# Optimization experiments

Measured on AMD Instinct MI355X. Metric: run time of the kernel, lower is better.

## Reference

```python
import jax, jax.numpy as jnp
import numpy as np

H, KB = 8, 8          # z_num grid (h, k)
OB, IB = 64, 64       # per-call weight block [OB, IB, K]
K, L = 9, 9           # kernel dims of exe_unet_weight and unet_1d_weights
ZD, PD, DH = 64, 16, 128  # z_dim, pde_inputs dim, hypernet hidden


def setup_inputs() -> dict:
    key = jax.random.key(0)
    k1, k2, k3, k4, k5 = jax.random.split(key, 5)
    # z params: torch.fmod(randn, 2) as in the original __init__
    z_all = jnp.fmod(jax.random.normal(k1, (H * KB, ZD), jnp.float32), 2.0)
    W1 = jax.random.normal(k2, (DH, ZD + PD), jnp.float32) * 0.1
    b1 = jnp.zeros((DH,), jnp.float32)
    W2 = jax.random.normal(k3, (OB * IB * K, DH), jnp.float32) * 0.02
    b2 = jnp.zeros((OB * IB * K,), jnp.float32)
    unet_1d_weights = jax.random.normal(k4, (H * OB, KB * IB, L), jnp.float32)
    pde_inputs = jax.random.normal(k5, (PD,), jnp.float32)
    return {"z_all": z_all, "W1": W1, "b1": b1, "W2": W2, "b2": b2,
            "unet_1d_weights": unet_1d_weights, "pde_inputs": pde_inputs}


def reference(z_all, W1, b1, W2, b2, unet_1d_weights, pde_inputs):
    # Batched hypernet: one GEMM over all h*k z vectors instead of h*k calls.
    x = jnp.concatenate([z_all, jnp.broadcast_to(pde_inputs, (H * KB, PD))], axis=1)  # [hk, ZD+PD]
    hid = jax.nn.relu(x @ W1.T + b1)                    # [hk, DH]
    w = (hid @ W2.T + b2).reshape(H, KB, OB, IB, K)      # per-cell blocks
    # cat(dim=1) within row, cat(dim=0) across rows -> [H*OB, KB*IB, K]
    exe_unet_weight = w.transpose(0, 2, 1, 3, 4).reshape(H * OB, KB * IB, K)
    # broadcast outer product over kernel dims
    w_2d = jnp.einsum('oik,oil->oikl', exe_unet_weight, unet_1d_weights)
    return w_2d
```

## Files before the change

kernel.cpp:

```cpp
#include <hip/hip_runtime.h>

#define ZD_ 64
#define PD_ 16
#define DH_ 128

__global__ void hid_kernel(const float* __restrict__ z_all,
                           const float* __restrict__ W1,
                           const float* __restrict__ b1,
                           const float* __restrict__ pde,
                           float* __restrict__ hid) {
    int gid = blockIdx.x * 256 + threadIdx.x;
    int r = gid >> 7;
    int d = gid & 127;
    const float* w = W1 + d * (ZD_ + PD_);
    const float* z = z_all + r * ZD_;
    float acc = b1[d];
    #pragma unroll 8
    for (int c = 0; c < ZD_; ++c) acc += z[c] * w[c];
    #pragma unroll
    for (int c = 0; c < PD_; ++c) acc += pde[c] * w[ZD_ + c];
    hid[gid] = fmaxf(acc, 0.0f);
}

__global__ __launch_bounds__(256, 4) void fused_kernel(
        const float* __restrict__ hid,
        const float* __restrict__ W2,
        const float* __restrict__ b2,
        const float* __restrict__ unet,
        float* __restrict__ out) {
    __shared__ __align__(16) float s_w2[36 * 132];
    __shared__ float s_exe[64 * 36];
    __shared__ float s_un [64 * 36];

    int tid = threadIdx.x;
    int b   = blockIdx.x;
    int ob  = b >> 4;
    int ibg = b & 15;
    int n0  = ob * 576 + ibg * 36;

    const float4* g4 = reinterpret_cast<const float4*>(W2 + (size_t)n0 * DH_);
    for (int j = tid; j < 1152; j += 256) {
        int row  = j >> 5;
        int col4 = j & 31;
        *reinterpret_cast<float4*>(&s_w2[row * 132 + col4 * 4]) = g4[j];
    }

    for (int idx = tid; idx < 2304; idx += 256) {
        int rr = idx / 36;
        int jj = idx - rr * 36;
        int h  = rr >> 3, kb = rr & 7;
        size_t ub = ((size_t)((h * 64 + ob) * 512 + kb * 64 + ibg * 4)) * 9;
        s_un[idx] = unet[ub + jj];
    }
    __syncthreads();

    int cell = tid >> 2;
    int ib   = tid & 3;
    const float4* h4p = reinterpret_cast<const float4*>(hid + cell * DH_);
    const float*  wb  = s_w2 + ib * 9 * 132;
    const float*  bp  = b2 + n0 + ib * 9;

    float acc[9];
    #pragma unroll
    for (int k = 0; k < 9; ++k) acc[k] = bp[k];

    #pragma unroll 4
    for (int c = 0; c < 32; ++c) {
        float4 h4 = h4p[c];
        #pragma unroll
        for (int k = 0; k < 9; ++k) {
            float4 w4 = *reinterpret_cast<const float4*>(wb + k * 132 + c * 4);
            acc[k] += h4.x * w4.x + h4.y * w4.y + h4.z * w4.z + h4.w * w4.w;
        }
    }
    #pragma unroll
    for (int k = 0; k < 9; ++k) s_exe[tid * 9 + k] = acc[k];
    __syncthreads();

    for (int idx = tid; idx < 5184; idx += 256) {
        int rr = idx / 81;
        int q  = idx - rr * 81;
        float4 v;
        float* vp = &v.x;
        #pragma unroll
        for (int j2 = 0; j2 < 4; ++j2) {
            int e   = q * 4 + j2;
            int ibb = e / 81;
            int rem = e - ibb * 81;
            int k   = rem / 9;
            int l   = rem - k * 9;
            vp[j2] = s_exe[rr * 36 + ibb * 9 + k] * s_un[rr * 36 + ibb * 9 + l];
        }
        int h = rr >> 3, kb = rr & 7;
        size_t base = ((size_t)((h * 64 + ob) * 512 + kb * 64 + ibg * 4)) * 81;
        reinterpret_cast<float4*>(out + base)[q] = v;
    }
}

extern "C" void kernel_launch(void* const* d_in, const int* in_sizes, int n_in,
                              void* d_out, int out_size, void* d_ws, size_t ws_size,
                              hipStream_t stream) {
    const float* z_all = (const float*)d_in[0];
    const float* W1    = (const float*)d_in[1];
    const float* b1    = (const float*)d_in[2];
    const float* W2    = (const float*)d_in[3];
    const float* b2    = (const float*)d_in[4];
    const float* unet  = (const float*)d_in[5];
    const float* pde   = (const float*)d_in[6];
    float* out = (float*)d_out;

    float* hid = (float*)d_ws;

    hid_kernel<<<32, 256, 0, stream>>>(z_all, W1, b1, pde, hid);
    fused_kernel<<<1024, 256, 0, stream>>>(hid, W2, b2, unet, out);
}
```

Baseline: 143.1 us.

## Keep hidden vectors in registers and read W2 rows wave-uniformly, doubling block tile

Result: slower. 219.7 us (+53.6%).

```diff
diff --git a/kernel.cpp b/kernel.cpp
--- a/kernel.cpp
+++ b/kernel.cpp
@@ -22,78 +22,87 @@
     hid[gid] = fmaxf(acc, 0.0f);
 }
 
-__global__ __launch_bounds__(256, 4) void fused_kernel(
+#define EXE_STRIDE 73
+#define UN_STRIDE  72
+
+__global__ __launch_bounds__(256) void fused_kernel(
         const float* __restrict__ hid,
         const float* __restrict__ W2,
         const float* __restrict__ b2,
         const float* __restrict__ unet,
         float* __restrict__ out) {
-    __shared__ __align__(16) float s_w2[36 * 132];
-    __shared__ float s_exe[64 * 36];
-    __shared__ float s_un [64 * 36];
+    __shared__ float s_exe[64 * EXE_STRIDE];
+    __shared__ __align__(16) float s_un[64 * UN_STRIDE];
 
-    int tid = threadIdx.x;
-    int b   = blockIdx.x;
-    int ob  = b >> 4;
-    int ibg = b & 15;
-    int n0  = ob * 576 + ibg * 36;
+    int tid  = threadIdx.x;
+    int b    = blockIdx.x;
+    int ob   = b >> 3;
+    int ibp  = b & 7;
+    int wave = __builtin_amdgcn_readfirstlane(tid >> 6);
+    int lane = tid & 63;
 
-    const float4* g4 = reinterpret_cast<const float4*>(W2 + (size_t)n0 * DH_);
+    float4 hreg[32];
+    const float4* hp = reinterpret_cast<const float4*>(hid + lane * DH_);
+    #pragma unroll
+    for (int c = 0; c < 32; ++c) hreg[c] = hp[c];
+
     for (int j = tid; j < 1152; j += 256) {
-        int row  = j >> 5;
-        int col4 = j & 31;
-        *reinterpret_cast<float4*>(&s_w2[row * 132 + col4 * 4]) = g4[j];
+        int cell = j / 18;
+        int q    = j - cell * 18;
+        int hh = cell >> 3, kk = cell & 7;
+        size_t gb = ((size_t)((hh * 64 + ob) * 512 + kk * 64 + ibp * 8)) * 9;
+        float4 v = *reinterpret_cast<const float4*>(unet + gb + q * 4);
+        *reinterpret_cast<float4*>(&s_un[cell * UN_STRIDE + q * 4]) = v;
     }
 
-    for (int idx = tid; idx < 2304; idx += 256) {
-        int rr = idx / 36;
-        int jj = idx - rr * 36;
-        int h  = rr >> 3, kb = rr & 7;
-        size_t ub = ((size_t)((h * 64 + ob) * 512 + kb * 64 + ibg * 4)) * 9;
-        s_un[idx] = unet[ub + jj];
+    #pragma unroll
+    for (int t = 0; t < 2; ++t) {
+        int ibl = wave + t * 4;
+        int n_base = __builtin_amdgcn_readfirstlane(
+                         ob * 576 + (ibp * 8 + ibl) * 9);
+        #pragma unroll
+        for (int k = 0; k < 9; ++k) {
+            const float* wrow = W2 + (size_t)(n_base + k) * DH_;
+            float a0 = 0.f, a1 = 0.f, a2 = 0.f, a3 = 0.f;
+            #pragma unroll
+            for (int c = 0; c < 32; c += 4) {
+                float4 w0 = *reinterpret_cast<const float4*>(wrow + c * 4);
+                float4 w1 = *reinterpret_cast<const float4*>(wrow + c * 4 + 4);
+                float4 w2 = *reinterpret_cast<const float4*>(wrow + c * 4 + 8);
+                float4 w3 = *reinterpret_cast<const float4*>(wrow + c * 4 + 12);
+                a0 += w0.x * hreg[c+0].x + w0.y * hreg[c+0].y
+                    + w0.z * hreg[c+0].z + w0.w * hreg[c+0].w;
+                a1 += w1.x * hreg[c+1].x + w1.y * hreg[c+1].y
+                    + w1.z * hreg[c+1].z + w1.w * hreg[c+1].w;
+                a2 += w2.x * hreg[c+2].x + w2.y * hreg[c+2].y
+                    + w2.z * hreg[c+2].z + w2.w * hreg[c+2].w;
+                a3 += w3.x * hreg[c+3].x + w3.y * hreg[c+3].y
+                    + w3.z * hreg[c+3].z + w3.w * hreg[c+3].w;
+            }
+            float acc = b2[n_base + k] + ((a0 + a1) + (a2 + a3));
+            s_exe[lane * EXE_STRIDE + ibl * 9 + k] = acc;
+        }
     }
     __syncthreads();
 
-    int cell = tid >> 2;
-    int ib   = tid & 3;
-    const float4* h4p = reinterpret_cast<const float4*>(hid + cell * DH_);
-    const float*  wb  = s_w2 + ib * 9 * 132;
-    const float*  bp  = b2 + n0 + ib * 9;
-
-    float acc[9];
-    #pragma unroll
-    for (int k = 0; k < 9; ++k) acc[k] = bp[k];
-
-    #pragma unroll 4
-    for (int c = 0; c < 32; ++c) {
-        float4 h4 = h4p[c];
-        #pragma unroll
-        for (int k = 0; k < 9; ++k) {
-            float4 w4 = *reinterpret_cast<const float4*>(wb + k * 132 + c * 4);
-            acc[k] += h4.x * w4.x + h4.y * w4.y + h4.z * w4.z + h4.w * w4.w;
-        }
-    }
-    #pragma unroll
-    for (int k = 0; k < 9; ++k) s_exe[tid * 9 + k] = acc[k];
-    __syncthreads();
-
-    for (int idx = tid; idx < 5184; idx += 256) {
-        int rr = idx / 81;
-        int q  = idx - rr * 81;
+    for (int idx = tid; idx < 10368; idx += 256) {
+        int cell = idx / 162;
+        int q    = idx - cell * 162;
         float4 v;
         float* vp = &v.x;
         #pragma unroll
         for (int j2 = 0; j2 < 4; ++j2) {
             int e   = q * 4 + j2;
-            int ibb = e / 81;
-            int rem = e - ibb * 81;
+            int ibl = e / 81;
+            int rem = e - ibl * 81;
             int k   = rem / 9;
             int l   = rem - k * 9;
-            vp[j2] = s_exe[rr * 36 + ibb * 9 + k] * s_un[rr * 36 + ibb * 9 + l];
+            vp[j2] = s_exe[cell * EXE_STRIDE + ibl * 9 + k]
+                   * s_un [cell * UN_STRIDE  + ibl * 9 + l];
         }
-        int h = rr >> 3, kb = rr & 7;
-        size_t base = ((size_t)((h * 64 + ob) * 512 + kb * 64 + ibg * 4)) * 81;
-        reinterpret_cast<float4*>(out + base)[q] = v;
+        int hh = cell >> 3, kk = cell & 7;
+        size_t gb = ((size_t)((hh * 64 + ob) * 512 + kk * 64 + ibp * 8)) * 81;
+        reinterpret_cast<float4*>(out + gb)[q] = v;
     }
 }
 
@@ -112,5 +121,5 @@
     float* hid = (float*)d_ws;
 
     hid_kernel<<<32, 256, 0, stream>>>(z_all, W1, b1, pde, hid);
-    fused_kernel<<<1024, 256, 0, stream>>>(hid, W2, b2, unet, out);
+    fused_kernel<<<512, 256, 0, stream>>>(hid, W2, b2, unet, out);
 }
```

## Retile hypernet GEMM with transposed hidden in LDS, split-K and wider blocks

Applied to the files above, without the earlier changes.

Measured after the change: 138.2 us, median of 2. -3.4%, faster.

```diff
diff --git a/kernel.cpp b/kernel.cpp
--- a/kernel.cpp
+++ b/kernel.cpp
@@ -8,10 +8,10 @@
                            const float* __restrict__ W1,
                            const float* __restrict__ b1,
                            const float* __restrict__ pde,
-                           float* __restrict__ hid) {
+                           float* __restrict__ hidT) {
     int gid = blockIdx.x * 256 + threadIdx.x;
-    int r = gid >> 7;
-    int d = gid & 127;
+    int d = gid >> 6;
+    int r = gid & 63;
     const float* w = W1 + d * (ZD_ + PD_);
     const float* z = z_all + r * ZD_;
     float acc = b1[d];
@@ -19,81 +19,134 @@
     for (int c = 0; c < ZD_; ++c) acc += z[c] * w[c];
     #pragma unroll
     for (int c = 0; c < PD_; ++c) acc += pde[c] * w[ZD_ + c];
-    hid[gid] = fmaxf(acc, 0.0f);
+    hidT[d * 64 + r] = fmaxf(acc, 0.0f);
 }
 
-__global__ __launch_bounds__(256, 4) void fused_kernel(
-        const float* __restrict__ hid,
+#define SMEM_FLOATS 18208
+
+__global__ __launch_bounds__(256) void fused_kernel(
+        const float* __restrict__ hidT,
         const float* __restrict__ W2,
         const float* __restrict__ b2,
         const float* __restrict__ unet,
         float* __restrict__ out) {
-    __shared__ __align__(16) float s_w2[36 * 132];
-    __shared__ float s_exe[64 * 36];
-    __shared__ float s_un [64 * 36];
+    __shared__ __align__(16) float smem[SMEM_FLOATS];
+    float* s_w2 = smem;
+    float* s_hT = smem + 9504;
 
     int tid = threadIdx.x;
     int b   = blockIdx.x;
-    int ob  = b >> 4;
-    int ibg = b & 15;
-    int n0  = ob * 576 + ibg * 36;
+    int ob  = b >> 3;
+    int ibp = b & 7;
+    int n0  = ob * 576 + ibp * 72;
 
     const float4* g4 = reinterpret_cast<const float4*>(W2 + (size_t)n0 * DH_);
-    for (int j = tid; j < 1152; j += 256) {
-        int row  = j >> 5;
-        int col4 = j & 31;
-        *reinterpret_cast<float4*>(&s_w2[row * 132 + col4 * 4]) = g4[j];
+    #pragma unroll
+    for (int t = 0; t < 9; ++t) {
+        int j   = t * 256 + tid;
+        int row = j >> 5;
+        int c4  = j & 31;
+        *reinterpret_cast<float4*>(&s_w2[row * 132 + c4 * 4]) = g4[j];
+    }
+    const float4* h4g = reinterpret_cast<const float4*>(hidT);
+    #pragma unroll
+    for (int t = 0; t < 8; ++t) {
+        int j  = t * 256 + tid;
+        int d  = j >> 4;
+        int r4 = j & 15;
+        *reinterpret_cast<float4*>(&s_hT[d * 68 + r4 * 4]) = h4g[j];
     }
 
-    for (int idx = tid; idx < 2304; idx += 256) {
-        int rr = idx / 36;
-        int jj = idx - rr * 36;
-        int h  = rr >> 3, kb = rr & 7;
-        size_t ub = ((size_t)((h * 64 + ob) * 512 + kb * 64 + ibg * 4)) * 9;
-        s_un[idx] = unet[ub + jj];
+    int cg  = tid & 15;
+    int ibl = (tid >> 4) & 7;
+    int ks  = tid >> 7;
+
+    float4 acc[9];
+    if (ks == 0) {
+        #pragma unroll
+        for (int kk = 0; kk < 9; ++kk) {
+            float bv = b2[n0 + ibl * 9 + kk];
+            acc[kk] = make_float4(bv, bv, bv, bv);
+        }
+    } else {
+        #pragma unroll
+        for (int kk = 0; kk < 9; ++kk) acc[kk] = make_float4(0.f, 0.f, 0.f, 0.f);
     }
     __syncthreads();
 
-    int cell = tid >> 2;
-    int ib   = tid & 3;
-    const float4* h4p = reinterpret_cast<const float4*>(hid + cell * DH_);
-    const float*  wb  = s_w2 + ib * 9 * 132;
-    const float*  bp  = b2 + n0 + ib * 9;
-
-    float acc[9];
-    #pragma unroll
-    for (int k = 0; k < 9; ++k) acc[k] = bp[k];
-
-    #pragma unroll 4
-    for (int c = 0; c < 32; ++c) {
-        float4 h4 = h4p[c];
+    const float* wbase = s_w2 + ibl * 9 * 132 + ks * 64;
+    const float* hbase = s_hT + (size_t)ks * 64 * 68 + 4 * cg;
+    #pragma unroll 2
+    for (int cc = 0; cc < 64; cc += 4) {
+        float4 h0 = *reinterpret_cast<const float4*>(&hbase[(cc + 0) * 68]);
+        float4 h1 = *reinterpret_cast<const float4*>(&hbase[(cc + 1) * 68]);
+        float4 h2 = *reinterpret_cast<const float4*>(&hbase[(cc + 2) * 68]);
+        float4 h3 = *reinterpret_cast<const float4*>(&hbase[(cc + 3) * 68]);
         #pragma unroll
-        for (int k = 0; k < 9; ++k) {
-            float4 w4 = *reinterpret_cast<const float4*>(wb + k * 132 + c * 4);
-            acc[k] += h4.x * w4.x + h4.y * w4.y + h4.z * w4.z + h4.w * w4.w;
+        for (int kk = 0; kk < 9; ++kk) {
+            float4 w = *reinterpret_cast<const float4*>(&wbase[kk * 132 + cc]);
+            acc[kk].x += h0.x * w.x + h1.x * w.y + h2.x * w.z + h3.x * w.w;
+            acc[kk].y += h0.y * w.x + h1.y * w.y + h2.y * w.z + h3.y * w.w;
+            acc[kk].z += h0.z * w.x + h1.z * w.y + h2.z * w.z + h3.z * w.w;
+            acc[kk].w += h0.w * w.x + h1.w * w.y + h2.w * w.z + h3.w * w.w;
         }
     }
-    #pragma unroll
-    for (int k = 0; k < 9; ++k) s_exe[tid * 9 + k] = acc[k];
     __syncthreads();
 
-    for (int idx = tid; idx < 5184; idx += 256) {
-        int rr = idx / 81;
-        int q  = idx - rr * 81;
+    float* s_exe = smem;
+    float* s_red = smem + 4672;
+    float* s_un  = smem + 9504;
+
+    if (ks == 1) {
+        int slot = tid & 127;
+        #pragma unroll
+        for (int kk = 0; kk < 9; ++kk) {
+            s_red[slot * 37 + 0 * 9 + kk] = acc[kk].x;
+            s_red[slot * 37 + 1 * 9 + kk] = acc[kk].y;
+            s_red[slot * 37 + 2 * 9 + kk] = acc[kk].z;
+            s_red[slot * 37 + 3 * 9 + kk] = acc[kk].w;
+        }
+    }
+    for (int j = tid; j < 1152; j += 256) {
+        int cell = j / 18;
+        int q    = j - cell * 18;
+        int hh = cell >> 3, kb = cell & 7;
+        size_t gb = ((size_t)((hh * 64 + ob) * 512 + kb * 64 + ibp * 8)) * 9;
+        *reinterpret_cast<float4*>(&s_un[cell * 72 + q * 4]) =
+            *reinterpret_cast<const float4*>(unet + gb + q * 4);
+    }
+    __syncthreads();
+
+    if (ks == 0) {
+        #pragma unroll
+        for (int kk = 0; kk < 9; ++kk) {
+            int col = ibl * 9 + kk;
+            s_exe[(4 * cg + 0) * 73 + col] = acc[kk].x + s_red[tid * 37 + 0 * 9 + kk];
+            s_exe[(4 * cg + 1) * 73 + col] = acc[kk].y + s_red[tid * 37 + 1 * 9 + kk];
+            s_exe[(4 * cg + 2) * 73 + col] = acc[kk].z + s_red[tid * 37 + 2 * 9 + kk];
+            s_exe[(4 * cg + 3) * 73 + col] = acc[kk].w + s_red[tid * 37 + 3 * 9 + kk];
+        }
+    }
+    __syncthreads();
+
+    for (int idx = tid; idx < 10368; idx += 256) {
+        int cell = idx / 162;
+        int q    = idx - cell * 162;
         float4 v;
         float* vp = &v.x;
         #pragma unroll
         for (int j2 = 0; j2 < 4; ++j2) {
-            int e   = q * 4 + j2;
-            int ibb = e / 81;
-            int rem = e - ibb * 81;
-            int k   = rem / 9;
-            int l   = rem - k * 9;
-            vp[j2] = s_exe[rr * 36 + ibb * 9 + k] * s_un[rr * 36 + ibb * 9 + l];
+            int e    = q * 4 + j2;
+            int ibl2 = e / 81;
+            int rem  = e - ibl2 * 81;
+            int k    = rem / 9;
+            int l    = rem - k * 9;
+            vp[j2] = s_exe[cell * 73 + ibl2 * 9 + k]
+                   * s_un [cell * 72 + ibl2 * 9 + l];
         }
-        int h = rr >> 3, kb = rr & 7;
-        size_t base = ((size_t)((h * 64 + ob) * 512 + kb * 64 + ibg * 4)) * 81;
-        reinterpret_cast<float4*>(out + base)[q] = v;
+        int hh = cell >> 3, kb = cell & 7;
+        size_t gb = ((size_t)((hh * 64 + ob) * 512 + kb * 64 + ibp * 8)) * 81;
+        reinterpret_cast<float4*>(out + gb)[q] = v;
     }
 }
 
@@ -109,8 +162,8 @@
     const float* pde   = (const float*)d_in[6];
     float* out = (float*)d_out;
 
-    float* hid = (float*)d_ws;
+    float* hidT = (float*)d_ws;
 
-    hid_kernel<<<32, 256, 0, stream>>>(z_all, W1, b1, pde, hid);
-    fused_kernel<<<1024, 256, 0, stream>>>(hid, W2, b2, unet, out);
+    hid_kernel<<<32, 256, 0, stream>>>(z_all, W1, b1, pde, hidT);
+    fused_kernel<<<512, 256, 0, stream>>>(hidT, W2, b2, unet, out);
 }
```
